# Optimization experiments

Hardware: AMD Instinct MI355X
Metric: run time of the kernel (lower is better)

The kernel has to match this reference:

```python
import jax, jax.numpy as jnp
import numpy as np

K = 5  # kernel_size, n_qubits = K*K = 25
PAD = (K - 1) // 2  # 'same' padding, stride 1


def _extract_patches(x):
    """x: [B, C, H, W] -> [B, C, H, W, K*K] 5x5 patches, zero 'same' padding."""
    B, C, H, W = x.shape
    xp = jnp.pad(x, ((0, 0), (0, 0), (PAD, PAD), (PAD, PAD)))
    # 25 static shifted views stacked on a trailing axis (fixed small loop)
    return jnp.stack(
        [xp[:, :, di:di + H, dj:dj + W] for di in range(K) for dj in range(K)],
        axis=-1,
    )


def _vqc_1mout(patches, w):
    """Analytic expectation <Z_0> of the vqc_1mout circuit:
    AngleEmbedding (RX) of the 25 patch values, one BasicEntanglerLayer
    (per-wire RX(w_i) followed by a CNOT ring 0->1->...->24->0), measure Z on
    wire 0. Heisenberg-propagating Z_0 through the CNOT ring gives the tensor
    product of Z on wires 1..24 over the product state after the RX rotations,
    so <Z_0> = prod_{i=1..24} cos(x_i + w_i).
    patches: [..., 25], w: [25] -> out: [...].
    """
    y = jnp.cos(patches + w)  # broadcast over trailing 25
    return jnp.prod(y[..., 1:], axis=-1)


def setup_inputs() -> dict:
    key = jax.random.key(0)
    kx, kw = jax.random.split(key)
    x = jax.random.normal(kx, (32, 16, 64, 64), dtype=jnp.float32)
    # learned VQC rotation angles (n_qlayers=1, 25 qubits)
    w = jax.random.uniform(kw, (K * K,), dtype=jnp.float32,
                           minval=0.0, maxval=2.0 * np.pi)
    return {"x": x, "w": w}


def reference(x, w):
    # depthwise quanvolution: out[b, f, h, w] = VQC(5x5 patch of x[b, f])
    patches = _extract_patches(x)          # [B, C, H, W, 25]
    return _vqc_1mout(patches, w)          # [B, C, H, W]
```

## Files before the change

kernel.cpp:

```cpp
#include <hip/hip_runtime.h>
#include <hip/hip_bf16.h>
#include <math.h>


#define TILE_ROWS 16
#define HALO 2
#define SM_ROWS (TILE_ROWS + 2 * HALO)
#define SM_COLS (64 + 2 * HALO)

__global__ __launch_bounds__(256, 4)
void qconv5x5_kernel(const float* __restrict__ x, const float* __restrict__ w,
                     float* __restrict__ out)
{
    __shared__ float2 sm[SM_ROWS][SM_COLS];
    __shared__ float2 smw[25];

    const int tid   = threadIdx.x;
    const int bid   = blockIdx.x;
    const int plane = bid >> 2;
    const int r0    = (bid & 3) * TILE_ROWS;

    const float* xp = x + plane * 64 * 64;

    if (tid < 25) {
        float s, c;
        __sincosf(w[tid], &s, &c);
        smw[tid] = make_float2(c, s);
    }

    for (int i = tid; i < SM_ROWS * SM_COLS; i += 256) {
        int rr = i / SM_COLS;
        int cc = i - rr * SM_COLS;
        int gr = r0 + rr - HALO;
        int gc = cc - HALO;
        float c = 1.0f, s = 0.0f;
        if ((unsigned)gr < 64u && (unsigned)gc < 64u) {
            __sincosf(xp[gr * 64 + gc], &s, &c);
        }
        sm[rr][cc] = make_float2(c, s);
    }
    __syncthreads();

    float cw[25], sw[25];
#pragma unroll
    for (int p = 0; p < 25; ++p) { cw[p] = smw[p].x; sw[p] = smw[p].y; }

    const int tx = tid & 63;
    const int q  = tid >> 6;

    float prod[4] = {1.f, 1.f, 1.f, 1.f};

#pragma unroll
    for (int nr = 0; nr < 8; ++nr) {
        const int tr = q * 4 + nr;
        float2 v[5];
#pragma unroll
        for (int dj = 0; dj < 5; ++dj) v[dj] = sm[tr][tx + dj];
#pragma unroll
        for (int ro = 0; ro < 4; ++ro) {
            const int di = nr - ro;
            if (di < 0 || di > 4) continue;
#pragma unroll
            for (int dj = 0; dj < 5; ++dj) {
                const int p = di * 5 + dj;
                if (p == 0) continue;
                prod[ro] *= fmaf(v[dj].x, cw[p], -(v[dj].y * sw[p]));
            }
        }
    }

    float* op = out + plane * 64 * 64 + (r0 + q * 4) * 64 + tx;
#pragma unroll
    for (int ro = 0; ro < 4; ++ro) op[ro * 64] = prod[ro];
}

extern "C" void kernel_launch(void* const* d_in, const int* in_sizes, int n_in,
                              void* d_out, int out_size, void* d_ws, size_t ws_size,
                              hipStream_t stream) {
    const float* x = (const float*)d_in[0];
    const float* w = (const float*)d_in[1];
    float* out = (float*)d_out;
    (void)in_sizes; (void)n_in; (void)out_size; (void)d_ws; (void)ws_size;

    const int planes = 32 * 16;
    dim3 grid(planes * (64 / TILE_ROWS));
    dim3 block(256);
    qconv5x5_kernel<<<grid, block, 0, stream>>>(x, w, out);
}
```

Before: 70.06 us.

## Double row tile to 32 rows with 8 outputs per thread and scalar weights

Doubles the row tile per block from 16 to 32, so each thread computes 8 output rows, which cuts halo recomputation of sincos and shared-memory row loads per output. Weight sincos moves from a shared-memory array to per-thread computation, broadcast through readfirstlane so the values can live in scalar registers, and the extra barrier dependency on the weight table goes away. The launch-bounds occupancy hint is dropped, and the larger tile halves the grid and raises register pressure from 8 accumulators.

Result: no change. 68.82 us (-1.8%).

```diff
diff --git a/kernel.cpp b/kernel.cpp
--- a/kernel.cpp
+++ b/kernel.cpp
@@ -3,36 +3,40 @@
 #include <math.h>
 
 
-#define TILE_ROWS 16
-#define HALO 2
-#define SM_ROWS (TILE_ROWS + 2 * HALO)
-#define SM_COLS (64 + 2 * HALO)
+#define TR   32
+#define SMR  (TR + 4)
+#define SMC  (64 + 4)
 
-__global__ __launch_bounds__(256, 4)
+__device__ __forceinline__ float uni(float v) {
+    return __uint_as_float(__builtin_amdgcn_readfirstlane(__float_as_uint(v)));
+}
+
+__global__ __launch_bounds__(256)
 void qconv5x5_kernel(const float* __restrict__ x, const float* __restrict__ w,
                      float* __restrict__ out)
 {
-    __shared__ float2 sm[SM_ROWS][SM_COLS];
-    __shared__ float2 smw[25];
+    __shared__ float2 sm[SMR][SMC];
 
     const int tid   = threadIdx.x;
     const int bid   = blockIdx.x;
-    const int plane = bid >> 2;
-    const int r0    = (bid & 3) * TILE_ROWS;
+    const int plane = bid >> 1;
+    const int r0    = (bid & 1) * TR;
+
+    float cw[25], sw[25];
+#pragma unroll
+    for (int p = 0; p < 25; ++p) {
+        float s, c;
+        __sincosf(w[p], &s, &c);
+        cw[p] = uni(c);
+        sw[p] = uni(s);
+    }
 
     const float* xp = x + plane * 64 * 64;
-
-    if (tid < 25) {
-        float s, c;
-        __sincosf(w[tid], &s, &c);
-        smw[tid] = make_float2(c, s);
-    }
-
-    for (int i = tid; i < SM_ROWS * SM_COLS; i += 256) {
-        int rr = i / SM_COLS;
-        int cc = i - rr * SM_COLS;
-        int gr = r0 + rr - HALO;
-        int gc = cc - HALO;
+    for (int i = tid; i < SMR * SMC; i += 256) {
+        const int rr = i / SMC;
+        const int cc = i - rr * SMC;
+        const int gr = r0 + rr - 2;
+        const int gc = cc - 2;
         float c = 1.0f, s = 0.0f;
         if ((unsigned)gr < 64u && (unsigned)gc < 64u) {
             __sincosf(xp[gr * 64 + gc], &s, &c);
@@ -41,23 +45,21 @@
     }
     __syncthreads();
 
-    float cw[25], sw[25];
-#pragma unroll
-    for (int p = 0; p < 25; ++p) { cw[p] = smw[p].x; sw[p] = smw[p].y; }
-
     const int tx = tid & 63;
     const int q  = tid >> 6;
 
-    float prod[4] = {1.f, 1.f, 1.f, 1.f};
+    float prod[8];
+#pragma unroll
+    for (int ro = 0; ro < 8; ++ro) prod[ro] = 1.0f;
 
 #pragma unroll
-    for (int nr = 0; nr < 8; ++nr) {
-        const int tr = q * 4 + nr;
+    for (int nr = 0; nr < 12; ++nr) {
+        const int tr = q * 8 + nr;
         float2 v[5];
 #pragma unroll
         for (int dj = 0; dj < 5; ++dj) v[dj] = sm[tr][tx + dj];
 #pragma unroll
-        for (int ro = 0; ro < 4; ++ro) {
+        for (int ro = 0; ro < 8; ++ro) {
             const int di = nr - ro;
             if (di < 0 || di > 4) continue;
 #pragma unroll
@@ -69,9 +71,9 @@
         }
     }
 
-    float* op = out + plane * 64 * 64 + (r0 + q * 4) * 64 + tx;
+    float* op = out + plane * 64 * 64 + (r0 + q * 8) * 64 + tx;
 #pragma unroll
-    for (int ro = 0; ro < 4; ++ro) op[ro * 64] = prod[ro];
+    for (int ro = 0; ro < 8; ++ro) op[ro * 64] = prod[ro];
 }
 
 extern "C" void kernel_launch(void* const* d_in, const int* in_sizes, int n_in,
@@ -83,7 +85,7 @@
     (void)in_sizes; (void)n_in; (void)out_size; (void)d_ws; (void)ws_size;
 
     const int planes = 32 * 16;
-    dim3 grid(planes * (64 / TILE_ROWS));
+    dim3 grid(planes * (64 / TR));
     dim3 block(256);
     qconv5x5_kernel<<<grid, block, 0, stream>>>(x, w, out);
 }
```
